# Kernel tuning notes

Hardware: AMD Instinct MI355X
Metric: run time of the kernel (lower is better)

## Reference

```python
import jax, jax.numpy as jnp
import numpy as np

INPUT_DIM = 16
HIDDEN = 64
N_RAW = INPUT_DIM - 3  # 13 raw features, last 3 are xyz coords


def setup_inputs() -> dict:
    key = jax.random.key(0)
    ks = jax.random.split(key, 16)
    B, N = 4, 512
    D = HIDDEN
    s = lambda fan_in: 1.0 / np.sqrt(fan_in)
    x = jax.random.normal(ks[0], (B, N, INPUT_DIM), dtype=jnp.float32)
    # feature projection [N_RAW -> D]
    Wf = jax.random.uniform(ks[1], (N_RAW, D), jnp.float32, -s(N_RAW), s(N_RAW))
    bf = jax.random.uniform(ks[2], (D,), jnp.float32, -s(N_RAW), s(N_RAW))
    # positional encoding MLP [3 -> D -> D]
    Wp1 = jax.random.uniform(ks[3], (3, D), jnp.float32, -s(3), s(3))
    bp1 = jax.random.uniform(ks[4], (D,), jnp.float32, -s(3), s(3))
    Wp2 = jax.random.uniform(ks[5], (D, D), jnp.float32, -s(D), s(D))
    bp2 = jax.random.uniform(ks[6], (D,), jnp.float32, -s(D), s(D))
    # node projection [D -> D]
    Wn = jax.random.uniform(ks[7], (D, D), jnp.float32, -s(D), s(D))
    bn = jax.random.uniform(ks[8], (D,), jnp.float32, -s(D), s(D))
    # edge MLP [2D -> D -> D//2 -> 1]
    W1 = jax.random.uniform(ks[9], (2 * D, D), jnp.float32, -s(2 * D), s(2 * D))
    b1 = jax.random.uniform(ks[10], (D,), jnp.float32, -s(2 * D), s(2 * D))
    W2 = jax.random.uniform(ks[11], (D, D // 2), jnp.float32, -s(D), s(D))
    b2 = jax.random.uniform(ks[12], (D // 2,), jnp.float32, -s(D), s(D))
    W3 = jax.random.uniform(ks[13], (D // 2, 1), jnp.float32, -s(D // 2), s(D // 2))
    b3 = jax.random.uniform(ks[14], (1,), jnp.float32, -s(D // 2), s(D // 2))
    return dict(x=x, Wf=Wf, bf=bf, Wp1=Wp1, bp1=bp1, Wp2=Wp2, bp2=bp2,
                Wn=Wn, bn=bn, W1=W1, b1=b1, W2=W2, b2=b2, W3=W3, b3=b3)


def reference(x, Wf, bf, Wp1, bp1, Wp2, bp2, Wn, bn, W1, b1, W2, b2, W3, b3):
    # split raw features / xyz coords
    feats = x[..., :N_RAW]           # [B,N,13]
    xyz = x[..., -3:]                # [B,N,3]
    pos = jax.nn.relu(xyz @ Wp1 + bp1) @ Wp2 + bp2
    proj = feats @ Wf + bf + pos     # [B,N,D]
    emb = proj @ Wn + bn             # [B,N,D] node embeddings
    # edge MLP layer1 on concat([u_i, u_j]): decompose W1 = [W1a; W1b].
    # cat([u_i,u_j]) @ W1 == u_i @ W1a + u_j @ W1b  (same math, no [B,N,N,2D])
    D = emb.shape[-1]
    a = emb @ W1[:D]                 # [B,N,D]
    b = emb @ W1[D:]                 # [B,N,D]
    h = jax.nn.relu(a[:, :, None, :] + b[:, None, :, :] + b1)  # [B,N,N,D]
    h = jax.nn.relu(h @ W2 + b2)     # [B,N,N,D//2]  (dropout = identity in eval)
    logits = (h @ W3 + b3)[..., 0]   # [B,N,N]
    return logits
```

## Files before the change

### kernel.cpp

```cpp
#include <hip/hip_runtime.h>
#include <stdint.h>

#define NPTS 512
#define NB 4
#define TJB 128
#define BST 72
#define SOST 40

typedef __attribute__((ext_vector_type(4))) float floatx4;
typedef __fp16 fp16x2 __attribute__((ext_vector_type(2)));
typedef _Float16 half2v __attribute__((ext_vector_type(2)));
typedef _Float16 half8v __attribute__((ext_vector_type(8)));

union H8 { fp16x2 p2[4]; half2v h2[4]; half8v h8; };

__global__ __launch_bounds__(256) void rows_kernel(
    const float* __restrict__ x,
    const float* __restrict__ Wf,  const float* __restrict__ bf,
    const float* __restrict__ Wp1, const float* __restrict__ bp1,
    const float* __restrict__ Wp2, const float* __restrict__ bp2,
    const float* __restrict__ Wn,  const float* __restrict__ bn,
    const float* __restrict__ W1,  const float* __restrict__ b1,
    _Float16* __restrict__ wsA, _Float16* __restrict__ wsB)
{
    __shared__ float posh[4][64];
    __shared__ float projS[4][64];
    __shared__ float embS[4][64];

    const int r   = threadIdx.x >> 6;
    const int t   = threadIdx.x & 63;
    const int row = blockIdx.x * 4 + r;
    const float* xr = x + row * 16;

    const float x13 = xr[13], x14 = xr[14], x15 = xr[15];
    float ph = x13 * Wp1[t] + x14 * Wp1[64 + t] + x15 * Wp1[128 + t] + bp1[t];
    posh[r][t] = fmaxf(ph, 0.f);
    __syncthreads();

    float s0 = 0.f, s1 = 0.f, s2 = 0.f, s3 = 0.f;
    #pragma unroll
    for (int k = 0; k < 64; k += 4) {
        s0 += posh[r][k    ] * Wp2[(k    ) * 64 + t];
        s1 += posh[r][k + 1] * Wp2[(k + 1) * 64 + t];
        s2 += posh[r][k + 2] * Wp2[(k + 2) * 64 + t];
        s3 += posh[r][k + 3] * Wp2[(k + 3) * 64 + t];
    }
    float acc = bp2[t] + ((s0 + s1) + (s2 + s3)) + bf[t];
    float f0 = 0.f, f1 = 0.f, f2 = 0.f, f3 = 0.f;
    #pragma unroll
    for (int k = 0; k < 12; k += 4) {
        f0 += xr[k    ] * Wf[(k    ) * 64 + t];
        f1 += xr[k + 1] * Wf[(k + 1) * 64 + t];
        f2 += xr[k + 2] * Wf[(k + 2) * 64 + t];
        f3 += xr[k + 3] * Wf[(k + 3) * 64 + t];
    }
    acc += ((f0 + f1) + (f2 + f3)) + xr[12] * Wf[12 * 64 + t];
    projS[r][t] = acc;
    __syncthreads();

    float e0 = 0.f, e1 = 0.f, e2 = 0.f, e3 = 0.f;
    #pragma unroll
    for (int k = 0; k < 64; k += 4) {
        e0 += projS[r][k    ] * Wn[(k    ) * 64 + t];
        e1 += projS[r][k + 1] * Wn[(k + 1) * 64 + t];
        e2 += projS[r][k + 2] * Wn[(k + 2) * 64 + t];
        e3 += projS[r][k + 3] * Wn[(k + 3) * 64 + t];
    }
    embS[r][t] = bn[t] + ((e0 + e1) + (e2 + e3));
    __syncthreads();

    float a0 = 0.f, a1 = 0.f, a2 = 0.f, a3 = 0.f;
    float v0 = 0.f, v1 = 0.f, v2 = 0.f, v3 = 0.f;
    #pragma unroll
    for (int k = 0; k < 64; k += 4) {
        const float g0 = embS[r][k], g1 = embS[r][k + 1], g2 = embS[r][k + 2], g3 = embS[r][k + 3];
        a0 += g0 * W1[(k    ) * 64 + t];
        a1 += g1 * W1[(k + 1) * 64 + t];
        a2 += g2 * W1[(k + 2) * 64 + t];
        a3 += g3 * W1[(k + 3) * 64 + t];
        v0 += g0 * W1[(64 + k    ) * 64 + t];
        v1 += g1 * W1[(64 + k + 1) * 64 + t];
        v2 += g2 * W1[(64 + k + 2) * 64 + t];
        v3 += g3 * W1[(64 + k + 3) * 64 + t];
    }
    wsA[row * 64 + t] = (_Float16)(b1[t] + ((a0 + a1) + (a2 + a3)));
    wsB[row * 64 + t] = (_Float16)((v0 + v1) + (v2 + v3));
}

__global__ __launch_bounds__(256) void pairs_kernel(
    const _Float16* __restrict__ wsA, const _Float16* __restrict__ wsB,
    const float* __restrict__ W2,  const float* __restrict__ b2,
    const float* __restrict__ W3,  const float* __restrict__ b3,
    float* __restrict__ out)
{
    __shared__ _Float16 bS[TJB][BST];
    __shared__ _Float16 sO[4][2][16][SOST];

    const int tid = threadIdx.x;
    const int w   = tid >> 6;
    const int l   = tid & 63;
    const int q   = l >> 4;
    const int c   = l & 15;
    const int q8  = q * 8;

    const int bidx = blockIdx.x;
    const int jt = bidx & 3;
    const int ig = (bidx >> 2) & 63;
    const int bb = bidx >> 8;
    const int j0 = jt * TJB;
    const int i0 = ig * 8 + w * 2;

    const _Float16* bG = wsB + (bb * NPTS + j0) * 64;
    #pragma unroll
    for (int p = 0; p < 4; ++p) {
        const int flat = p * 256 + tid;
        const int rr = flat >> 3, ch = (flat & 7) * 8;
        *(half8v*)&bS[rr][ch] = *(const half8v*)(bG + rr * 64 + ch);
    }

    half8v Wf16[2][2];
    #pragma unroll
    for (int kt = 0; kt < 2; ++kt)
        #pragma unroll
        for (int nt = 0; nt < 2; ++nt) {
            H8 u;
            #pragma unroll
            for (int e = 0; e < 8; ++e)
                u.h8[e] = (_Float16)W2[(kt * 32 + q8 + e) * 32 + nt * 16 + c];
            Wf16[kt][nt] = u.h8;
        }

    half8v w3f;
    #pragma unroll
    for (int e = 0; e < 8; ++e) {
        const int p = q8 + e;
        w3f[e] = (_Float16)W3[(p >> 1) + ((p & 1) << 4)];
    }

    const float b2c = b2[c], b2c16 = b2[c + 16];
    const float b3v = b3[0];

    const _Float16* aG0 = wsA + (bb * NPTS + i0) * 64;
    const _Float16* aG1 = aG0 + 64;
    const half8v aA0 = *(const half8v*)(aG0 + q8);
    const half8v aA1 = *(const half8v*)(aG0 + 32 + q8);
    const half8v aB0 = *(const half8v*)(aG1 + q8);
    const half8v aB1 = *(const half8v*)(aG1 + 32 + q8);
    const half8v zero8 = (half8v)(_Float16)0.0f;

    __syncthreads();

    float* orow0 = out + ((size_t)(bb * NPTS + i0)) * NPTS + j0;
    float* orow1 = orow0 + NPTS;

    #pragma unroll 2
    for (int mt = 0; mt < 8; ++mt) {
        const int m = mt * 16 + c;
        const half8v b0v = *(const half8v*)&bS[m][q8];
        const half8v b1v = *(const half8v*)&bS[m][32 + q8];

        const half8v hA0 = __builtin_elementwise_max(aA0 + b0v, zero8);
        const half8v hA1 = __builtin_elementwise_max(aA1 + b1v, zero8);
        const half8v hB0 = __builtin_elementwise_max(aB0 + b0v, zero8);
        const half8v hB1 = __builtin_elementwise_max(aB1 + b1v, zero8);

        floatx4 aA0c = {b2c, b2c, b2c, b2c};
        floatx4 aA1c = {b2c16, b2c16, b2c16, b2c16};
        floatx4 aB0c = aA0c, aB1c = aA1c;
        aA0c = __builtin_amdgcn_mfma_f32_16x16x32_f16(hA0, Wf16[0][0], aA0c, 0, 0, 0);
        aA0c = __builtin_amdgcn_mfma_f32_16x16x32_f16(hA1, Wf16[1][0], aA0c, 0, 0, 0);
        aA1c = __builtin_amdgcn_mfma_f32_16x16x32_f16(hA0, Wf16[0][1], aA1c, 0, 0, 0);
        aA1c = __builtin_amdgcn_mfma_f32_16x16x32_f16(hA1, Wf16[1][1], aA1c, 0, 0, 0);
        aB0c = __builtin_amdgcn_mfma_f32_16x16x32_f16(hB0, Wf16[0][0], aB0c, 0, 0, 0);
        aB0c = __builtin_amdgcn_mfma_f32_16x16x32_f16(hB1, Wf16[1][0], aB0c, 0, 0, 0);
        aB1c = __builtin_amdgcn_mfma_f32_16x16x32_f16(hB0, Wf16[0][1], aB1c, 0, 0, 0);
        aB1c = __builtin_amdgcn_mfma_f32_16x16x32_f16(hB1, Wf16[1][1], aB1c, 0, 0, 0);

        #pragma unroll
        for (int r = 0; r < 4; ++r) {
            H8 pkA, pkB;
            pkA.p2[0] = __builtin_amdgcn_cvt_pkrtz(aA0c[r], aA1c[r]);
            pkA.h2[0] = __builtin_elementwise_max(pkA.h2[0], (half2v)(_Float16)0.0f);
            *(half2v*)&sO[w][0][q * 4 + r][2 * c] = pkA.h2[0];
            pkB.p2[0] = __builtin_amdgcn_cvt_pkrtz(aB0c[r], aB1c[r]);
            pkB.h2[0] = __builtin_elementwise_max(pkB.h2[0], (half2v)(_Float16)0.0f);
            *(half2v*)&sO[w][1][q * 4 + r][2 * c] = pkB.h2[0];
        }
        const half8v arA = *(const half8v*)&sO[w][0][c][q8];
        const half8v arB = *(const half8v*)&sO[w][1][c][q8];

        floatx4 dlA = {b3v, b3v, b3v, b3v};
        floatx4 dlB = {b3v, b3v, b3v, b3v};
        dlA = __builtin_amdgcn_mfma_f32_16x16x32_f16(arA, w3f, dlA, 0, 0, 0);
        dlB = __builtin_amdgcn_mfma_f32_16x16x32_f16(arB, w3f, dlB, 0, 0, 0);

        const float lgA = (c == 0) ? dlA[0] : ((c == 1) ? dlA[1] : ((c == 2) ? dlA[2] : dlA[3]));
        const float lgB = (c == 0) ? dlB[0] : ((c == 1) ? dlB[1] : ((c == 2) ? dlB[2] : dlB[3]));
        if (c < 4) {
            orow0[mt * 16 + q * 4 + c] = lgA;
            orow1[mt * 16 + q * 4 + c] = lgB;
        }
    }
}

extern "C" void kernel_launch(void* const* d_in, const int* in_sizes, int n_in,
                              void* d_out, int out_size, void* d_ws, size_t ws_size,
                              hipStream_t stream) {
    const float* x   = (const float*)d_in[0];
    const float* Wf  = (const float*)d_in[1];
    const float* bf  = (const float*)d_in[2];
    const float* Wp1 = (const float*)d_in[3];
    const float* bp1 = (const float*)d_in[4];
    const float* Wp2 = (const float*)d_in[5];
    const float* bp2 = (const float*)d_in[6];
    const float* Wn  = (const float*)d_in[7];
    const float* bn  = (const float*)d_in[8];
    const float* W1  = (const float*)d_in[9];
    const float* b1  = (const float*)d_in[10];
    const float* W2  = (const float*)d_in[11];
    const float* b2  = (const float*)d_in[12];
    const float* W3  = (const float*)d_in[13];
    const float* b3  = (const float*)d_in[14];

    _Float16* wsA = (_Float16*)d_ws;
    _Float16* wsB = wsA + NB * NPTS * 64;

    rows_kernel<<<NB * NPTS / 4, 256, 0, stream>>>(
        x, Wf, bf, Wp1, bp1, Wp2, bp2, Wn, bn, W1, b1, wsA, wsB);

    pairs_kernel<<<NB * 64 * 4, 256, 0, stream>>>(
        wsA, wsB, W2, b2, W3, b3, (float*)d_out);
}
```

Measured before the change: 96.76 us.

## Split rows kernel reductions across warps per row and unroll pair loop further

```diff
diff --git a/kernel.cpp b/kernel.cpp
--- a/kernel.cpp
+++ b/kernel.cpp
@@ -23,68 +23,79 @@
     const float* __restrict__ W1,  const float* __restrict__ b1,
     _Float16* __restrict__ wsA, _Float16* __restrict__ wsB)
 {
-    __shared__ float posh[4][64];
-    __shared__ float projS[4][64];
-    __shared__ float embS[4][64];
-
-    const int r   = threadIdx.x >> 6;
+    __shared__ float poshS[64];
+    __shared__ float projS[64];
+    __shared__ float embS[64];
+    __shared__ float partA[4][64];
+    __shared__ float partB[4][64];
+
     const int t   = threadIdx.x & 63;
-    const int row = blockIdx.x * 4 + r;
+    const int w   = threadIdx.x >> 6;
+    const int k0  = w * 16;
+    const int row = blockIdx.x;
     const float* xr = x + row * 16;
 
-    const float x13 = xr[13], x14 = xr[14], x15 = xr[15];
-    float ph = x13 * Wp1[t] + x14 * Wp1[64 + t] + x15 * Wp1[128 + t] + bp1[t];
-    posh[r][t] = fmaxf(ph, 0.f);
-    __syncthreads();
-
-    float s0 = 0.f, s1 = 0.f, s2 = 0.f, s3 = 0.f;
-    #pragma unroll
-    for (int k = 0; k < 64; k += 4) {
-        s0 += posh[r][k    ] * Wp2[(k    ) * 64 + t];
-        s1 += posh[r][k + 1] * Wp2[(k + 1) * 64 + t];
-        s2 += posh[r][k + 2] * Wp2[(k + 2) * 64 + t];
-        s3 += posh[r][k + 3] * Wp2[(k + 3) * 64 + t];
-    }
-    float acc = bp2[t] + ((s0 + s1) + (s2 + s3)) + bf[t];
-    float f0 = 0.f, f1 = 0.f, f2 = 0.f, f3 = 0.f;
-    #pragma unroll
-    for (int k = 0; k < 12; k += 4) {
-        f0 += xr[k    ] * Wf[(k    ) * 64 + t];
-        f1 += xr[k + 1] * Wf[(k + 1) * 64 + t];
-        f2 += xr[k + 2] * Wf[(k + 2) * 64 + t];
-        f3 += xr[k + 3] * Wf[(k + 3) * 64 + t];
-    }
-    acc += ((f0 + f1) + (f2 + f3)) + xr[12] * Wf[12 * 64 + t];
-    projS[r][t] = acc;
-    __syncthreads();
-
-    float e0 = 0.f, e1 = 0.f, e2 = 0.f, e3 = 0.f;
-    #pragma unroll
-    for (int k = 0; k < 64; k += 4) {
-        e0 += projS[r][k    ] * Wn[(k    ) * 64 + t];
-        e1 += projS[r][k + 1] * Wn[(k + 1) * 64 + t];
-        e2 += projS[r][k + 2] * Wn[(k + 2) * 64 + t];
-        e3 += projS[r][k + 3] * Wn[(k + 3) * 64 + t];
-    }
-    embS[r][t] = bn[t] + ((e0 + e1) + (e2 + e3));
-    __syncthreads();
-
-    float a0 = 0.f, a1 = 0.f, a2 = 0.f, a3 = 0.f;
-    float v0 = 0.f, v1 = 0.f, v2 = 0.f, v3 = 0.f;
-    #pragma unroll
-    for (int k = 0; k < 64; k += 4) {
-        const float g0 = embS[r][k], g1 = embS[r][k + 1], g2 = embS[r][k + 2], g3 = embS[r][k + 3];
-        a0 += g0 * W1[(k    ) * 64 + t];
-        a1 += g1 * W1[(k + 1) * 64 + t];
-        a2 += g2 * W1[(k + 2) * 64 + t];
-        a3 += g3 * W1[(k + 3) * 64 + t];
-        v0 += g0 * W1[(64 + k    ) * 64 + t];
-        v1 += g1 * W1[(64 + k + 1) * 64 + t];
-        v2 += g2 * W1[(64 + k + 2) * 64 + t];
-        v3 += g3 * W1[(64 + k + 3) * 64 + t];
-    }
-    wsA[row * 64 + t] = (_Float16)(b1[t] + ((a0 + a1) + (a2 + a3)));
-    wsB[row * 64 + t] = (_Float16)((v0 + v1) + (v2 + v3));
+    if (w == 0) {
+        const float x13 = xr[13], x14 = xr[14], x15 = xr[15];
+        float ph = x13 * Wp1[t] + x14 * Wp1[64 + t] + x15 * Wp1[128 + t] + bp1[t];
+        poshS[t] = fmaxf(ph, 0.f);
+    }
+    __syncthreads();
+
+    {
+        float s0 = 0.f, s1 = 0.f;
+        #pragma unroll
+        for (int k = 0; k < 16; k += 2) {
+            s0 += poshS[k0 + k    ] * Wp2[(k0 + k    ) * 64 + t];
+            s1 += poshS[k0 + k + 1] * Wp2[(k0 + k + 1) * 64 + t];
+        }
+        float p = s0 + s1;
+        if (w < 3) {
+            #pragma unroll
+            for (int k = 0; k < 4; ++k) p += xr[w * 4 + k] * Wf[(w * 4 + k) * 64 + t];
+        } else {
+            p += xr[12] * Wf[12 * 64 + t] + bf[t] + bp2[t];
+        }
+        partA[w][t] = p;
+    }
+    __syncthreads();
+
+    if (w == 0) projS[t] = (partA[0][t] + partA[1][t]) + (partA[2][t] + partA[3][t]);
+    __syncthreads();
+
+    {
+        float s0 = 0.f, s1 = 0.f;
+        #pragma unroll
+        for (int k = 0; k < 16; k += 2) {
+            s0 += projS[k0 + k    ] * Wn[(k0 + k    ) * 64 + t];
+            s1 += projS[k0 + k + 1] * Wn[(k0 + k + 1) * 64 + t];
+        }
+        partB[w][t] = s0 + s1 + ((w == 0) ? bn[t] : 0.f);
+    }
+    __syncthreads();
+
+    if (w == 0) embS[t] = (partB[0][t] + partB[1][t]) + (partB[2][t] + partB[3][t]);
+    __syncthreads();
+
+    {
+        float sa0 = 0.f, sa1 = 0.f, sb0 = 0.f, sb1 = 0.f;
+        #pragma unroll
+        for (int k = 0; k < 16; k += 2) {
+            const float g0 = embS[k0 + k], g1 = embS[k0 + k + 1];
+            sa0 += g0 * W1[(k0 + k    ) * 64 + t];
+            sa1 += g1 * W1[(k0 + k + 1) * 64 + t];
+            sb0 += g0 * W1[(64 + k0 + k    ) * 64 + t];
+            sb1 += g1 * W1[(64 + k0 + k + 1) * 64 + t];
+        }
+        partA[w][t] = sa0 + sa1 + ((w == 0) ? b1[t] : 0.f);
+        partB[w][t] = sb0 + sb1;
+    }
+    __syncthreads();
+
+    if (w == 0)
+        wsA[row * 64 + t] = (_Float16)((partA[0][t] + partA[1][t]) + (partA[2][t] + partA[3][t]));
+    else if (w == 1)
+        wsB[row * 64 + t] = (_Float16)((partB[0][t] + partB[1][t]) + (partB[2][t] + partB[3][t]));
 }
 
 __global__ __launch_bounds__(256) void pairs_kernel(
@@ -153,7 +164,7 @@
     float* orow0 = out + ((size_t)(bb * NPTS + i0)) * NPTS + j0;
     float* orow1 = orow0 + NPTS;
 
-    #pragma unroll 2
+    #pragma unroll 4
     for (int mt = 0; mt < 8; ++mt) {
         const int m = mt * 16 + c;
         const half8v b0v = *(const half8v*)&bS[m][q8];
@@ -225,7 +236,7 @@
     _Float16* wsA = (_Float16*)d_ws;
     _Float16* wsB = wsA + NB * NPTS * 64;
 
-    rows_kernel<<<NB * NPTS / 4, 256, 0, stream>>>(
+    rows_kernel<<<NB * NPTS, 256, 0, stream>>>(
         x, Wf, bf, Wp1, bp1, Wp2, bp2, Wn, bn, W1, b1, wsA, wsB);
 
     pairs_kernel<<<NB * 64 * 4, 256, 0, stream>>>(
```

After: 96.77 us. About the same (+0.0%).
